# Performance work log

Measured on AMD Instinct MI355X. Metric: run time of the kernel, lower is better.

## Reference

```python
import jax, jax.numpy as jnp
import numpy as np

N_SRC = 8192
N_DST = 8192
E = 524288
D = 128
M = 64


def layer_norm(x, g, b, eps=1e-5):
    mu = x.mean(-1, keepdims=True)
    var = ((x - mu) ** 2).mean(-1, keepdims=True)
    return (x - mu) * jax.lax.rsqrt(var + eps) * g + b


def setup_inputs() -> dict:
    key = jax.random.key(0)
    ks = jax.random.split(key, 32)

    def p(k, shape, s=0.02):
        return jax.random.normal(k, shape, jnp.float32) * s

    inp = {
        "src_embed": jax.random.normal(ks[0], (N_SRC, D), jnp.float32),
        "dst_embed": jax.random.normal(ks[1], (N_DST, D), jnp.float32),
        "v_s2d": jax.random.normal(ks[2], (E, M), jnp.float32),
        "v_d2s": jax.random.normal(ks[3], (E, M), jnp.float32),
        "e_s2d_dst": jax.random.randint(ks[4], (E,), 0, N_DST, jnp.int32),
        "e_d2s_dst": jax.random.randint(ks[5], (E,), 0, N_SRC, jnp.int32),
        # node transforms
        "W_src": p(ks[6], (D, D)), "b_src": jnp.zeros((D,), jnp.float32),
        "W_dst": p(ks[7], (D, D)), "b_dst": jnp.zeros((D,), jnp.float32),
        # edge-message transforms
        "W_sm": p(ks[8], (M, D)), "b_sm": jnp.zeros((D,), jnp.float32),
        "W_dm": p(ks[9], (M, D)), "b_dm": jnp.zeros((D,), jnp.float32),
        # apply_row: LNLayer (Linear+LayerNorm) then Linear
        "row_W1": p(ks[10], (D, D)), "row_b1": jnp.zeros((D,), jnp.float32),
        "row_g": jnp.ones((D,), jnp.float32), "row_beta": jnp.zeros((D,), jnp.float32),
        "row_W2": p(ks[11], (D, D)), "row_b2": jnp.zeros((D,), jnp.float32),
        # apply_col
        "col_W1": p(ks[12], (D, D)), "col_b1": jnp.zeros((D,), jnp.float32),
        "col_g": jnp.ones((D,), jnp.float32), "col_beta": jnp.zeros((D,), jnp.float32),
        "col_W2": p(ks[13], (D, D)), "col_b2": jnp.zeros((D,), jnp.float32),
    }
    return inp


def reference(src_embed, dst_embed, v_s2d, v_d2s, e_s2d_dst, e_d2s_dst,
              W_src, b_src, W_dst, b_dst, W_sm, b_sm, W_dm, b_dm,
              row_W1, row_b1, row_g, row_beta, row_W2, row_b2,
              col_W1, col_b1, col_g, col_beta, col_W2, col_b2):
    # node transforms: h[ntype]
    h_src = src_embed @ W_src + b_src          # [N_src, D]
    h_dst = dst_embed @ W_dst + b_dst          # [N_dst, D]
    # edge message transforms
    msg_s2d = v_s2d @ W_sm + b_sm              # [E, D]
    msg_d2s = v_d2s @ W_dm + b_dm              # [E, D]
    # message = h[dst-of-edge] * msg, scatter-sum onto destination nodes
    out_dst = jax.ops.segment_sum(h_dst[e_s2d_dst] * msg_s2d, e_s2d_dst,
                                  num_segments=N_DST)   # src2dst -> dst nodes
    out_src = jax.ops.segment_sum(h_src[e_d2s_dst] * msg_d2s, e_d2s_dst,
                                  num_segments=N_SRC)   # dst2src -> src nodes
    # residual apply: x + Linear(LayerNorm(Linear(out)))
    row = src_embed + (layer_norm(out_src @ row_W1 + row_b1, row_g, row_beta) @ row_W2 + row_b2)
    col = dst_embed + (layer_norm(out_dst @ col_W1 + col_b1, col_g, col_beta) @ col_W2 + col_b2)
    return row, col
```

## Files before the change

kernel.cpp:

```cpp
#include <hip/hip_runtime.h>


#define DEV __device__ __forceinline__

typedef __bf16 bf16x8 __attribute__((ext_vector_type(8)));
typedef unsigned short u16x8 __attribute__((ext_vector_type(8)));
typedef float f32x4 __attribute__((ext_vector_type(4)));

constexpr int N_NODES = 8192;
constexpr int NUM_E   = 524288;
constexpr int D       = 128;
constexpr int M       = 64;
constexpr int R       = 16;

DEV unsigned short f2bf(float f) {
    unsigned int x = __float_as_uint(f);
    unsigned int r = (x + 0x7fffu + ((x >> 16) & 1u)) >> 16;
    return (unsigned short)r;
}
DEV bf16x8 load8(const unsigned short* p) {
    return *reinterpret_cast<const bf16x8*>(p);
}
DEV bf16x8 cvt8(const float* p) {
    union { u16x8 u; bf16x8 b; } cv;
#pragma unroll
    for (int i = 0; i < 8; ++i) cv.u[i] = f2bf(p[i]);
    return cv.b;
}
DEV f32x4 mfma16(bf16x8 a, bf16x8 b, f32x4 c) {
    return __builtin_amdgcn_mfma_f32_16x16x32_bf16(a, b, c, 0, 0, 0);
}

struct TransArgs {
    const float* src[8];
    unsigned short* dst[8];
    int K[8];
};
__global__ __launch_bounds__(256) void transpose_k(TransArgs ta, int* __restrict__ counts) {
    int b = blockIdx.x;
    if (b >= 8) {
        int z = b - 8;
        int4 zero = {0, 0, 0, 0};
        int4* p = reinterpret_cast<int4*>(counts) + (size_t)z * 2048 + threadIdx.x;
#pragma unroll
        for (int q = 0; q < 8; ++q) p[q * 256] = zero;
        return;
    }
    const float* s = ta.src[b];
    unsigned short* d = ta.dst[b];
    int K = ta.K[b];
    int total = K << 7;
    for (int i = threadIdx.x; i < total; i += 256) {
        int k = i >> 7, n = i & 127;
        d[n * K + k] = f2bf(s[i]);
    }
}

__global__ __launch_bounds__(256) void hist_k(const int* __restrict__ i0,
                                              const int* __restrict__ i1,
                                              int* __restrict__ counts) {
    int t = blockIdx.x * 256 + threadIdx.x;
    int rep = blockIdx.x & (R - 1);
    int base = rep * N_NODES;
    const int4* p = (const int4*)i0;
    if (t >= NUM_E / 4) { p = (const int4*)i1; base += R * N_NODES; t -= NUM_E / 4; }
    int4 e = p[t];
    atomicAdd(counts + base + (e.x & (N_NODES - 1)), 1);
    atomicAdd(counts + base + (e.y & (N_NODES - 1)), 1);
    atomicAdd(counts + base + (e.z & (N_NODES - 1)), 1);
    atomicAdd(counts + base + (e.w & (N_NODES - 1)), 1);
}

__global__ __launch_bounds__(256) void reduce_k(const int* __restrict__ counts,
                                                int* __restrict__ cur_rel,
                                                int* __restrict__ tot) {
    int n = blockIdx.x * 256 + threadIdx.x;
    int dir = n >> 13;
    int node = n & (N_NODES - 1);
    const int* c = counts + (size_t)dir * R * N_NODES + node;
    int* cr = cur_rel + (size_t)dir * R * N_NODES + node;
    int s = 0;
#pragma unroll
    for (int r = 0; r < R; ++r) {
        int v = c[r * N_NODES];
        cr[r * N_NODES] = s;
        s += v;
    }
    tot[n] = s;
}

__global__ __launch_bounds__(256) void scan_k(const int* __restrict__ tot,
                                              int* __restrict__ offsets) {
    __shared__ int part[256];
    int t = threadIdx.x;
    int dir = blockIdx.x;
    const int* tt = tot + dir * N_NODES;
    int* off = offsets + dir * (N_NODES + 1);
    int local[32];
    int s = 0;
#pragma unroll
    for (int i = 0; i < 32; ++i) { int v = tt[t * 32 + i]; local[i] = s; s += v; }
    part[t] = s;
    __syncthreads();
    for (int dd = 1; dd < 256; dd <<= 1) {
        int w = (t >= dd) ? part[t - dd] : 0;
        __syncthreads();
        part[t] += w;
        __syncthreads();
    }
    int base = part[t] - s;
#pragma unroll
    for (int i = 0; i < 32; ++i) off[t * 32 + i] = base + local[i];
    if (t == 255) off[N_NODES] = part[255];
}

__global__ __launch_bounds__(256) void scatter_k(const int* __restrict__ i0,
                                                 const int* __restrict__ i1,
                                                 const int* __restrict__ offsets,
                                                 int* __restrict__ cur_rel,
                                                 int* __restrict__ csr) {
    int t = blockIdx.x * 256 + threadIdx.x;
    int rep = blockIdx.x & (R - 1);
    int dir = 0;
    if (t >= NUM_E / 4) { dir = 1; t -= NUM_E / 4; }
    const int4* idx = (const int4*)(dir ? i1 : i0);
    int4 nn = idx[t];
    const int* off = offsets + dir * (N_NODES + 1);
    int* cr = cur_rel + (size_t)dir * R * N_NODES + rep * N_NODES;
    int* c = csr + dir * NUM_E;
    int e = t * 4;
    int a = nn.x & (N_NODES - 1), b = nn.y & (N_NODES - 1);
    int cc = nn.z & (N_NODES - 1), d = nn.w & (N_NODES - 1);
    c[off[a] + atomicAdd(cr + a, 1)] = e;
    c[off[b] + atomicAdd(cr + b, 1)] = e + 1;
    c[off[cc] + atomicAdd(cr + cc, 1)] = e + 2;
    c[off[d] + atomicAdd(cr + d, 1)] = e + 3;
}

__global__ __launch_bounds__(256) void gather_k(const float* __restrict__ v0,
                                                const float* __restrict__ v1,
                                                const int* __restrict__ offsets,
                                                const int* __restrict__ csr,
                                                unsigned short* __restrict__ Ab) {
    int gw = (blockIdx.x * 256 + threadIdx.x) >> 6;
    int dir = gw >> 13;
    int n = gw & (N_NODES - 1);
    const float* v = dir ? v1 : v0;
    const int* off = offsets + dir * (N_NODES + 1);
    const int* cs = csr + dir * NUM_E;
    unsigned short* A = Ab + (size_t)dir * N_NODES * M;

    int lane = threadIdx.x & 63;
    const int f16 = lane & 15;
    const int g = lane >> 4;
    int j0 = off[n], j1 = off[n + 1];
    int rem = j1 - j0;
    f32x4 acc = {0.f, 0.f, 0.f, 0.f};

    int nfull = rem >> 5;
    int j = j0;
    if (nfull > 0) {
        int ia[8];
#pragma unroll
        for (int q = 0; q < 8; ++q) ia[q] = cs[j + g + q * 4];
        for (int it = 0; it < nfull; ++it) {
            int jn = j + 32;
            int pa[8];
            if ((it + 1) < nfull) {
#pragma unroll
                for (int q = 0; q < 8; ++q) pa[q] = cs[jn + g + q * 4];
            } else {
#pragma unroll
                for (int q = 0; q < 8; ++q) pa[q] = 0;
            }
            f32x4 d[8];
#pragma unroll
            for (int q = 0; q < 8; ++q)
                d[q] = *(const f32x4*)(v + (size_t)ia[q] * M + f16 * 4);
#pragma unroll
            for (int q = 0; q < 8; ++q) acc += d[q];
#pragma unroll
            for (int q = 0; q < 8; ++q) ia[q] = pa[q];
            j = jn;
        }
    }
    if (rem & 16) {
        int ia[4];
#pragma unroll
        for (int q = 0; q < 4; ++q) ia[q] = cs[j + g + q * 4];
        f32x4 d[4];
#pragma unroll
        for (int q = 0; q < 4; ++q)
            d[q] = *(const f32x4*)(v + (size_t)ia[q] * M + f16 * 4);
#pragma unroll
        for (int q = 0; q < 4; ++q) acc += d[q];
        j += 16;
    }
    for (; j < j1; j += 4) {
        int e = j + g;
        if (e < j1) acc += *(const f32x4*)(v + (size_t)cs[e] * M + f16 * 4);
    }
#pragma unroll
    for (int i = 0; i < 4; ++i) {
        acc[i] += __shfl_xor(acc[i], 16, 64);
        acc[i] += __shfl_xor(acc[i], 32, 64);
    }
    if (g == 0) {
        union { unsigned short u[4]; unsigned long long ll; } w;
#pragma unroll
        for (int i = 0; i < 4; ++i) w.u[i] = f2bf(acc[i]);
        *reinterpret_cast<unsigned long long*>(A + (size_t)n * M + f16 * 4) = w.ll;
    }
}

struct SideArgs {
    const float* X;
    const unsigned short* Wnode_t;
    const float* bnode;
    const unsigned short* Abf;
    const int* counts;
    const unsigned short* Wmsg_t;
    const float* bmsg;
    const unsigned short* W1_t;
    const float* b1;
    const float* g;
    const float* beta;
    const unsigned short* W2_t;
    const float* b2;
    float* out;
};

__global__ __launch_bounds__(256) void apply_k(SideArgs A0, SideArgs A1) {
    const int side = blockIdx.x >> 9;
    const SideArgs& a = side ? A1 : A0;
    const int grp = blockIdx.x & 511;
    const int nb = grp * 16;
    const int w = threadIdx.x >> 6;
    const int lane = threadIdx.x & 63;
    const int m = lane & 15;
    const int quad = lane >> 4;

    __shared__ __align__(16) unsigned short sP[16 * 136];
    __shared__ float part_s[4][16], part_sq[4][16];

    bf16x8 af[4];
#pragma unroll
    for (int ks = 0; ks < 4; ++ks)
        af[ks] = cvt8(a.X + (size_t)(nb + m) * D + ks * 32 + quad * 8);
    f32x4 acc_h[2] = {{0.f, 0.f, 0.f, 0.f}, {0.f, 0.f, 0.f, 0.f}};
#pragma unroll
    for (int i = 0; i < 2; ++i) {
        int dt = 2 * w + i;
#pragma unroll
        for (int ks = 0; ks < 4; ++ks) {
            bf16x8 bfr = load8(a.Wnode_t + (size_t)(dt * 16 + m) * D + ks * 32 + quad * 8);
            acc_h[i] = mfma16(af[ks], bfr, acc_h[i]);
        }
    }
    bf16x8 at[2];
#pragma unroll
    for (int ks = 0; ks < 2; ++ks)
        at[ks] = load8(a.Abf + (size_t)(nb + m) * M + ks * 32 + quad * 8);
    f32x4 acc_t[2] = {{0.f, 0.f, 0.f, 0.f}, {0.f, 0.f, 0.f, 0.f}};
#pragma unroll
    for (int i = 0; i < 2; ++i) {
        int dt = 2 * w + i;
#pragma unroll
        for (int ks = 0; ks < 2; ++ks) {
            bf16x8 bfr = load8(a.Wmsg_t + (size_t)(dt * 16 + m) * M + ks * 32 + quad * 8);
            acc_t[i] = mfma16(at[ks], bfr, acc_t[i]);
        }
    }
    {
        float cnt_f[4];
#pragma unroll
        for (int r = 0; r < 4; ++r) cnt_f[r] = (float)a.counts[nb + quad * 4 + r];
#pragma unroll
        for (int i = 0; i < 2; ++i) {
            int dt = 2 * w + i;
            float bn = a.bnode[dt * 16 + m];
            float bm = a.bmsg[dt * 16 + m];
#pragma unroll
            for (int r = 0; r < 4; ++r) {
                float hv = acc_h[i][r] + bn;
                float tv = acc_t[i][r] + cnt_f[r] * bm;
                sP[(quad * 4 + r) * 136 + dt * 16 + m] = f2bf(hv * tv);
            }
        }
    }
    __syncthreads();
    bf16x8 au[4];
#pragma unroll
    for (int ks = 0; ks < 4; ++ks)
        au[ks] = load8(sP + m * 136 + ks * 32 + quad * 8);
    f32x4 acc_u[2] = {{0.f, 0.f, 0.f, 0.f}, {0.f, 0.f, 0.f, 0.f}};
#pragma unroll
    for (int i = 0; i < 2; ++i) {
        int dt = 2 * w + i;
#pragma unroll
        for (int ks = 0; ks < 4; ++ks) {
            bf16x8 bfr = load8(a.W1_t + (size_t)(dt * 16 + m) * D + ks * 32 + quad * 8);
            acc_u[i] = mfma16(au[ks], bfr, acc_u[i]);
        }
    }
    float g_f[2], beta_f[2];
#pragma unroll
    for (int i = 0; i < 2; ++i) {
        int dt = 2 * w + i;
        float b1v = a.b1[dt * 16 + m];
        g_f[i] = a.g[dt * 16 + m];
        beta_f[i] = a.beta[dt * 16 + m];
#pragma unroll
        for (int r = 0; r < 4; ++r) acc_u[i][r] += b1v;
    }
    float s[4], sq[4];
#pragma unroll
    for (int r = 0; r < 4; ++r) { s[r] = 0.f; sq[r] = 0.f; }
#pragma unroll
    for (int i = 0; i < 2; ++i)
#pragma unroll
        for (int r = 0; r < 4; ++r) { float u = acc_u[i][r]; s[r] += u; sq[r] += u * u; }
#pragma unroll
    for (int off = 1; off < 16; off <<= 1) {
#pragma unroll
        for (int r = 0; r < 4; ++r) {
            s[r] += __shfl_xor(s[r], off, 64);
            sq[r] += __shfl_xor(sq[r], off, 64);
        }
    }
    if (m == 0) {
#pragma unroll
        for (int r = 0; r < 4; ++r) {
            part_s[w][quad * 4 + r] = s[r];
            part_sq[w][quad * 4 + r] = sq[r];
        }
    }
    __syncthreads();
    float mu[4], rstd[4];
#pragma unroll
    for (int r = 0; r < 4; ++r) {
        int node = quad * 4 + r;
        float S = part_s[0][node] + part_s[1][node] + part_s[2][node] + part_s[3][node];
        float SQ = part_sq[0][node] + part_sq[1][node] + part_sq[2][node] + part_sq[3][node];
        mu[r] = S * (1.0f / 128.0f);
        float var = SQ * (1.0f / 128.0f) - mu[r] * mu[r];
        rstd[r] = rsqrtf(fmaxf(var, 0.f) + 1e-5f);
    }
#pragma unroll
    for (int i = 0; i < 2; ++i) {
        int dt = 2 * w + i;
#pragma unroll
        for (int r = 0; r < 4; ++r) {
            float ln = (acc_u[i][r] - mu[r]) * rstd[r] * g_f[i] + beta_f[i];
            sP[(quad * 4 + r) * 136 + dt * 16 + m] = f2bf(ln);
        }
    }
    __syncthreads();
    bf16x8 ay[4];
#pragma unroll
    for (int ks = 0; ks < 4; ++ks)
        ay[ks] = load8(sP + m * 136 + ks * 32 + quad * 8);
    f32x4 acc_y[2] = {{0.f, 0.f, 0.f, 0.f}, {0.f, 0.f, 0.f, 0.f}};
#pragma unroll
    for (int i = 0; i < 2; ++i) {
        int dt = 2 * w + i;
#pragma unroll
        for (int ks = 0; ks < 4; ++ks) {
            bf16x8 bfr = load8(a.W2_t + (size_t)(dt * 16 + m) * D + ks * 32 + quad * 8);
            acc_y[i] = mfma16(ay[ks], bfr, acc_y[i]);
        }
    }
#pragma unroll
    for (int i = 0; i < 2; ++i) {
        int dt = 2 * w + i;
        float b2v = a.b2[dt * 16 + m];
#pragma unroll
        for (int r = 0; r < 4; ++r) {
            int node = nb + quad * 4 + r;
            int d = dt * 16 + m;
            float xv = a.X[(size_t)node * D + d];
            a.out[(size_t)node * D + d] = acc_y[i][r] + b2v + xv;
        }
    }
}

extern "C" void kernel_launch(void* const* d_in, const int* in_sizes, int n_in,
                              void* d_out, int out_size, void* d_ws, size_t ws_size,
                              hipStream_t stream) {
    const float* src_embed = (const float*)d_in[0];
    const float* dst_embed = (const float*)d_in[1];
    const float* v_s2d = (const float*)d_in[2];
    const float* v_d2s = (const float*)d_in[3];
    const int* e_s2d = (const int*)d_in[4];
    const int* e_d2s = (const int*)d_in[5];
    const float* W_src = (const float*)d_in[6];
    const float* b_src = (const float*)d_in[7];
    const float* W_dst = (const float*)d_in[8];
    const float* b_dst = (const float*)d_in[9];
    const float* W_sm = (const float*)d_in[10];
    const float* b_sm = (const float*)d_in[11];
    const float* W_dm = (const float*)d_in[12];
    const float* b_dm = (const float*)d_in[13];
    const float* row_W1 = (const float*)d_in[14];
    const float* row_b1 = (const float*)d_in[15];
    const float* row_g = (const float*)d_in[16];
    const float* row_beta = (const float*)d_in[17];
    const float* row_W2 = (const float*)d_in[18];
    const float* row_b2 = (const float*)d_in[19];
    const float* col_W1 = (const float*)d_in[20];
    const float* col_b1 = (const float*)d_in[21];
    const float* col_g = (const float*)d_in[22];
    const float* col_beta = (const float*)d_in[23];
    const float* col_W2 = (const float*)d_in[24];
    const float* col_b2 = (const float*)d_in[25];
    float* out = (float*)d_out;

    char* ws = (char*)d_ws;
    int* counts = (int*)(ws + 0);
    int* offsets = (int*)(ws + 1048576);
    int* cur_rel = (int*)(ws + 1114368);
    int* tot = (int*)(ws + 2162944);
    unsigned short* Wt = (unsigned short*)(ws + 2228480);
    unsigned short* Abf = (unsigned short*)(ws + 2457856);
    int* csr = (int*)(out + (size_t)N_NODES * D);

    TransArgs ta;
    const float* srcs[8] = {W_src, W_dst, W_sm, W_dm, row_W1, row_W2, col_W1, col_W2};
    int Ks[8] = {128, 128, 64, 64, 128, 128, 128, 128};
    int offs[8] = {0, 16384, 32768, 40960, 49152, 65536, 81920, 98304};
    for (int i = 0; i < 8; ++i) { ta.src[i] = srcs[i]; ta.dst[i] = Wt + offs[i]; ta.K[i] = Ks[i]; }
    transpose_k<<<40, 256, 0, stream>>>(ta, counts);

    hist_k<<<(2 * NUM_E / 4) / 256, 256, 0, stream>>>(e_s2d, e_d2s, counts);
    reduce_k<<<(2 * N_NODES) / 256, 256, 0, stream>>>(counts, cur_rel, tot);
    scan_k<<<2, 256, 0, stream>>>(tot, offsets);
    scatter_k<<<(2 * NUM_E / 4) / 256, 256, 0, stream>>>(e_s2d, e_d2s, offsets, cur_rel, csr);

    gather_k<<<(2 * N_NODES * 64) / 256, 256, 0, stream>>>(
        v_s2d, v_d2s, offsets, csr, Abf);

    SideArgs rowA = {src_embed, Wt + 0, b_src, Abf + (size_t)N_NODES * M, tot + N_NODES,
                     Wt + 40960, b_dm, Wt + 49152, row_b1, row_g, row_beta, Wt + 65536, row_b2,
                     out};
    SideArgs colA = {dst_embed, Wt + 16384, b_dst, Abf, tot,
                     Wt + 32768, b_sm, Wt + 81920, col_b1, col_g, col_beta, Wt + 98304, col_b2,
                     out + (size_t)N_NODES * D};
    apply_k<<<1024, 256, 0, stream>>>(rowA, colA);
}
```

Before: 467.7 us.

## Fuse per-node edge gather into apply kernel via shared-memory staging

Removes the separate gather kernel and has each apply block gather and sum the edge features for its 16 nodes directly into shared memory as bf16, then feed them to the message MFMA. This avoids a kernel launch and a global round-trip of the aggregated feature matrix. In exchange, the gather now runs on only 1024 blocks with a shallower unroll (16 edges per iteration instead of 32), which reduces memory-level parallelism for the latency-bound random gathers. The CSR buffer also moves from the output area into the workspace.

```diff
diff --git a/kernel.cpp b/kernel.cpp
--- a/kernel.cpp
+++ b/kernel.cpp
@@ -137,87 +137,13 @@
     c[off[d] + atomicAdd(cr + d, 1)] = e + 3;
 }
 
-__global__ __launch_bounds__(256) void gather_k(const float* __restrict__ v0,
-                                                const float* __restrict__ v1,
-                                                const int* __restrict__ offsets,
-                                                const int* __restrict__ csr,
-                                                unsigned short* __restrict__ Ab) {
-    int gw = (blockIdx.x * 256 + threadIdx.x) >> 6;
-    int dir = gw >> 13;
-    int n = gw & (N_NODES - 1);
-    const float* v = dir ? v1 : v0;
-    const int* off = offsets + dir * (N_NODES + 1);
-    const int* cs = csr + dir * NUM_E;
-    unsigned short* A = Ab + (size_t)dir * N_NODES * M;
-
-    int lane = threadIdx.x & 63;
-    const int f16 = lane & 15;
-    const int g = lane >> 4;
-    int j0 = off[n], j1 = off[n + 1];
-    int rem = j1 - j0;
-    f32x4 acc = {0.f, 0.f, 0.f, 0.f};
-
-    int nfull = rem >> 5;
-    int j = j0;
-    if (nfull > 0) {
-        int ia[8];
-#pragma unroll
-        for (int q = 0; q < 8; ++q) ia[q] = cs[j + g + q * 4];
-        for (int it = 0; it < nfull; ++it) {
-            int jn = j + 32;
-            int pa[8];
-            if ((it + 1) < nfull) {
-#pragma unroll
-                for (int q = 0; q < 8; ++q) pa[q] = cs[jn + g + q * 4];
-            } else {
-#pragma unroll
-                for (int q = 0; q < 8; ++q) pa[q] = 0;
-            }
-            f32x4 d[8];
-#pragma unroll
-            for (int q = 0; q < 8; ++q)
-                d[q] = *(const f32x4*)(v + (size_t)ia[q] * M + f16 * 4);
-#pragma unroll
-            for (int q = 0; q < 8; ++q) acc += d[q];
-#pragma unroll
-            for (int q = 0; q < 8; ++q) ia[q] = pa[q];
-            j = jn;
-        }
-    }
-    if (rem & 16) {
-        int ia[4];
-#pragma unroll
-        for (int q = 0; q < 4; ++q) ia[q] = cs[j + g + q * 4];
-        f32x4 d[4];
-#pragma unroll
-        for (int q = 0; q < 4; ++q)
-            d[q] = *(const f32x4*)(v + (size_t)ia[q] * M + f16 * 4);
-#pragma unroll
-        for (int q = 0; q < 4; ++q) acc += d[q];
-        j += 16;
-    }
-    for (; j < j1; j += 4) {
-        int e = j + g;
-        if (e < j1) acc += *(const f32x4*)(v + (size_t)cs[e] * M + f16 * 4);
-    }
-#pragma unroll
-    for (int i = 0; i < 4; ++i) {
-        acc[i] += __shfl_xor(acc[i], 16, 64);
-        acc[i] += __shfl_xor(acc[i], 32, 64);
-    }
-    if (g == 0) {
-        union { unsigned short u[4]; unsigned long long ll; } w;
-#pragma unroll
-        for (int i = 0; i < 4; ++i) w.u[i] = f2bf(acc[i]);
-        *reinterpret_cast<unsigned long long*>(A + (size_t)n * M + f16 * 4) = w.ll;
-    }
-}
-
 struct SideArgs {
     const float* X;
+    const float* v;
+    const int* off;
+    const int* cs;
     const unsigned short* Wnode_t;
     const float* bnode;
-    const unsigned short* Abf;
     const int* counts;
     const unsigned short* Wmsg_t;
     const float* bmsg;
@@ -240,8 +166,57 @@
     const int m = lane & 15;
     const int quad = lane >> 4;
 
+    __shared__ __align__(16) unsigned short sA[16 * 72];
     __shared__ __align__(16) unsigned short sP[16 * 136];
     __shared__ float part_s[4][16], part_sq[4][16];
+
+    {
+        const int f16 = lane & 15;
+        const int g = lane >> 4;
+        for (int nd = 0; nd < 4; ++nd) {
+            int n = nb + 4 * w + nd;
+            int j0 = a.off[n], j1 = a.off[n + 1];
+            f32x4 acc = {0.f, 0.f, 0.f, 0.f};
+            int nfull = (j1 - j0) >> 4;
+            int j = j0;
+            if (nfull > 0) {
+                int i0 = a.cs[j + g], i1 = a.cs[j + g + 4];
+                int i2 = a.cs[j + g + 8], i3 = a.cs[j + g + 12];
+                for (int it = 0; it < nfull; ++it) {
+                    int jn = j + 16;
+                    int p0 = 0, p1 = 0, p2 = 0, p3 = 0;
+                    if ((it + 1) < nfull) {
+                        p0 = a.cs[jn + g];
+                        p1 = a.cs[jn + g + 4];
+                        p2 = a.cs[jn + g + 8];
+                        p3 = a.cs[jn + g + 12];
+                    }
+                    f32x4 d0 = *(const f32x4*)(a.v + (size_t)i0 * M + f16 * 4);
+                    f32x4 d1 = *(const f32x4*)(a.v + (size_t)i1 * M + f16 * 4);
+                    f32x4 d2 = *(const f32x4*)(a.v + (size_t)i2 * M + f16 * 4);
+                    f32x4 d3 = *(const f32x4*)(a.v + (size_t)i3 * M + f16 * 4);
+                    acc += d0; acc += d1; acc += d2; acc += d3;
+                    i0 = p0; i1 = p1; i2 = p2; i3 = p3;
+                    j = jn;
+                }
+            }
+            for (; j < j1; j += 4) {
+                int e = j + g;
+                if (e < j1) acc += *(const f32x4*)(a.v + (size_t)a.cs[e] * M + f16 * 4);
+            }
+#pragma unroll
+            for (int i = 0; i < 4; ++i) {
+                acc[i] += __shfl_xor(acc[i], 16, 64);
+                acc[i] += __shfl_xor(acc[i], 32, 64);
+            }
+            if (g == 0) {
+                union { unsigned short u[4]; unsigned long long ll; } wv;
+#pragma unroll
+                for (int i = 0; i < 4; ++i) wv.u[i] = f2bf(acc[i]);
+                *reinterpret_cast<unsigned long long*>(sA + (4 * w + nd) * 72 + f16 * 4) = wv.ll;
+            }
+        }
+    }
 
     bf16x8 af[4];
 #pragma unroll
@@ -257,10 +232,12 @@
             acc_h[i] = mfma16(af[ks], bfr, acc_h[i]);
         }
     }
+    __syncthreads();
+
     bf16x8 at[2];
 #pragma unroll
     for (int ks = 0; ks < 2; ++ks)
-        at[ks] = load8(a.Abf + (size_t)(nb + m) * M + ks * 32 + quad * 8);
+        at[ks] = load8(sA + m * 72 + ks * 32 + quad * 8);
     f32x4 acc_t[2] = {{0.f, 0.f, 0.f, 0.f}, {0.f, 0.f, 0.f, 0.f}};
 #pragma unroll
     for (int i = 0; i < 2; ++i) {
@@ -421,8 +398,7 @@
     int* cur_rel = (int*)(ws + 1114368);
     int* tot = (int*)(ws + 2162944);
     unsigned short* Wt = (unsigned short*)(ws + 2228480);
-    unsigned short* Abf = (unsigned short*)(ws + 2457856);
-    int* csr = (int*)(out + (size_t)N_NODES * D);
+    int* csr = (int*)(ws + 2457856);
 
     TransArgs ta;
     const float* srcs[8] = {W_src, W_dst, W_sm, W_dm, row_W1, row_W2, col_W1, col_W2};
@@ -436,13 +412,12 @@
     scan_k<<<2, 256, 0, stream>>>(tot, offsets);
     scatter_k<<<(2 * NUM_E / 4) / 256, 256, 0, stream>>>(e_s2d, e_d2s, offsets, cur_rel, csr);
 
-    gather_k<<<(2 * N_NODES * 64) / 256, 256, 0, stream>>>(
-        v_s2d, v_d2s, offsets, csr, Abf);
-
-    SideArgs rowA = {src_embed, Wt + 0, b_src, Abf + (size_t)N_NODES * M, tot + N_NODES,
+    SideArgs rowA = {src_embed, v_d2s, offsets + (N_NODES + 1), csr + NUM_E,
+                     Wt + 0, b_src, tot + N_NODES,
                      Wt + 40960, b_dm, Wt + 49152, row_b1, row_g, row_beta, Wt + 65536, row_b2,
                      out};
-    SideArgs colA = {dst_embed, Wt + 16384, b_dst, Abf, tot,
+    SideArgs colA = {dst_embed, v_s2d, offsets, csr,
+                     Wt + 16384, b_dst, tot,
                      Wt + 32768, b_sm, Wt + 81920, col_b1, col_g, col_beta, Wt + 98304, col_b2,
                      out + (size_t)N_NODES * D};
     apply_k<<<1024, 256, 0, stream>>>(rowA, colA);
```

New measurement: 464.2 us. About the same (-0.7%).
